# Optimization experiments

Hardware: AMD Instinct MI355X
Metric: run time of the kernel (lower is better)

## Reference

```python
import jax, jax.numpy as jnp
import numpy as np

N = 20000      # nodes
E = 640000     # edges (before self-loops)
NFEAT = 512
NHID = 128
HEADS = 2
NOUT = 64
K = 100
ALPHA = 0.2          # LeakyReLU negative slope
CLUSTER_TEMP = 5.0


def gat_layer(x, W, a_src, a_dst, b, src, dst, n, heads, out_c, neg_slope):
    """PyG-style GATConv (eval mode, self-loops already in src/dst).
    W: [heads*out_c, in_c], a_src/a_dst: [heads, out_c], b: [heads*out_c]."""
    h = (x @ W.T).reshape(n, heads, out_c)               # [N,H,C]
    alpha_src = (h * a_src[None]).sum(-1)                # [N,H]
    alpha_dst = (h * a_dst[None]).sum(-1)                # [N,H]
    e = alpha_src[src] + alpha_dst[dst]                  # [E',H]
    e = jnp.where(e > 0, e, neg_slope * e)               # LeakyReLU
    # segment softmax over incoming edges of each dst node
    m = jax.ops.segment_max(e, dst, num_segments=n)
    ex = jnp.exp(e - m[dst])
    s = jax.ops.segment_sum(ex, dst, num_segments=n)
    a = ex / (s[dst] + 1e-16)                            # [E',H]
    out = jax.ops.segment_sum(h[src] * a[:, :, None], dst, num_segments=n)
    return out.reshape(n, heads * out_c) + b


def cluster_iter(data_n, mu, num_iter, cluster_temp):
    """Soft k-means on row-normalized data. data_n: [N,D], mu: [K,D]."""
    def body(mu, _):
        dist = data_n @ mu.T                              # [N,K]
        r = jax.nn.softmax(cluster_temp * dist, axis=1)
        cluster_r = r.sum(axis=0)                         # [K]
        cluster_mean = r.T @ data_n                       # [K,D]
        return cluster_mean / cluster_r[:, None], None
    mu, _ = jax.lax.scan(body, mu, None, length=num_iter)
    dist = data_n @ mu.T
    r = jax.nn.softmax(cluster_temp * dist, axis=1)
    return mu, r, dist


def setup_inputs() -> dict:
    key = jax.random.key(0)
    ks = jax.random.split(key, 12)
    x = jax.random.normal(ks[0], (N, NFEAT), dtype=jnp.float32)
    edge_index = jax.random.randint(ks[1], (2, E), 0, N, dtype=jnp.int32)
    # GATConv layer 1 params
    W1 = jax.random.normal(ks[2], (HEADS * NHID, NFEAT), dtype=jnp.float32) * 0.05
    a_src1 = jax.random.normal(ks[3], (HEADS, NHID), dtype=jnp.float32) * 0.1
    a_dst1 = jax.random.normal(ks[4], (HEADS, NHID), dtype=jnp.float32) * 0.1
    b1 = jnp.zeros((HEADS * NHID,), dtype=jnp.float32)
    # GATConv layer 2 params (heads=1)
    W2 = jax.random.normal(ks[5], (NOUT, HEADS * NHID), dtype=jnp.float32) * 0.05
    a_src2 = jax.random.normal(ks[6], (1, NOUT), dtype=jnp.float32) * 0.1
    a_dst2 = jax.random.normal(ks[7], (1, NOUT), dtype=jnp.float32) * 0.1
    b2 = jnp.zeros((NOUT,), dtype=jnp.float32)
    # cluster init (self.init = torch.rand(K, nout))
    mu0 = jax.random.uniform(ks[8], (K, NOUT), dtype=jnp.float32)
    return {"x": x, "W1": W1, "a_src1": a_src1, "a_dst1": a_dst1, "b1": b1,
            "W2": W2, "a_src2": a_src2, "a_dst2": a_dst2, "b2": b2,
            "mu0": mu0, "edge_index": edge_index, "num_iter": 10}


def reference(x, W1, a_src1, a_dst1, b1, W2, a_src2, a_dst2, b2, mu0,
              edge_index, num_iter):
    loops = jnp.arange(N, dtype=edge_index.dtype)
    src = jnp.concatenate([edge_index[0], loops])
    dst = jnp.concatenate([edge_index[1], loops])
    h = jax.nn.elu(gat_layer(x, W1, a_src1, a_dst1, b1, src, dst,
                             N, HEADS, NHID, ALPHA))
    embeds = gat_layer(h, W2, a_src2, a_dst2, b2, src, dst,
                       N, 1, NOUT, ALPHA) + 1e-6
    data_n = embeds / jnp.linalg.norm(embeds, axis=1, keepdims=True)
    mu_init, _, _ = cluster_iter(data_n, mu0, num_iter, CLUSTER_TEMP)
    mu, r, dist = cluster_iter(data_n, jax.lax.stop_gradient(mu_init), 1,
                               CLUSTER_TEMP)
    return mu, r, embeds, dist
```

## Files before the change

### kernel.cpp

```cpp
#include <hip/hip_runtime.h>
#include <math.h>

#define Nn 20000
#define Ee 640000
#define ETOT 660000
#define NF 512
#define C1 256
#define C2 64
#define KC 100
#define TEMP 5.0f
#define NSLOPE 0.2f
#define NPART 250
#define CHB 80

__device__ __forceinline__ float wredSum(float v) {
#pragma unroll
  for (int off = 32; off > 0; off >>= 1) v += __shfl_xor(v, off, 64);
  return v;
}
__device__ __forceinline__ float wredMax(float v) {
#pragma unroll
  for (int off = 32; off > 0; off >>= 1) v = fmaxf(v, __shfl_xor(v, off, 64));
  return v;
}

__global__ void hist_kernel(const int* __restrict__ ei, int* __restrict__ deg) {
  int e = blockIdx.x * 256 + threadIdx.x;
  if (e >= ETOT) return;
  int dst = e < Ee ? ei[Ee + e] : e - Ee;
  atomicAdd(&deg[dst], 1);
}

__global__ __launch_bounds__(1024) void scan2_kernel(const int* __restrict__ deg,
    int* __restrict__ rowp, int* __restrict__ curs) {
  __shared__ int wsum[16];
  __shared__ int wpre[16];
  int t = threadIdx.x;
  int lane = t & 63, w = t >> 6;
  int loc[20];
  int tot = 0;
  int base = t * 20;
  if (t < 1000) {
#pragma unroll
    for (int i = 0; i < 20; i++) { tot += deg[base + i]; loc[i] = tot; }
  }
  int s = tot;
#pragma unroll
  for (int off = 1; off < 64; off <<= 1) {
    int u = __shfl_up(s, off, 64);
    if (lane >= off) s += u;
  }
  if (lane == 63) wsum[w] = s;
  __syncthreads();
  if (t == 0) {
    int c = 0;
#pragma unroll
    for (int i = 0; i < 16; i++) { c += wsum[i]; wpre[i] = c; }
    rowp[0] = 0;
  }
  __syncthreads();
  int p = (w > 0 ? wpre[w - 1] : 0) + s - tot;
  if (t < 1000) {
    int prev = 0;
#pragma unroll
    for (int i = 0; i < 20; i++) {
      rowp[base + i + 1] = p + loc[i];
      curs[base + i] = p + prev;
      prev = loc[i];
    }
  }
}

__global__ void scatter_kernel(const int* __restrict__ ei, int* __restrict__ curs,
                               int* __restrict__ ssort, int* __restrict__ dsort) {
  int e = blockIdx.x * 256 + threadIdx.x;
  if (e >= ETOT) return;
  int src = e < Ee ? ei[e] : e - Ee;
  int dst = e < Ee ? ei[Ee + e] : e - Ee;
  int pos = atomicAdd(&curs[dst], 1);
  ssort[pos] = src;
  dsort[pos] = dst;
}

__global__ __launch_bounds__(256) void edge_e1(const int* __restrict__ ssort,
    const int* __restrict__ dsort, const float* __restrict__ asn,
    const float* __restrict__ adn, float2* __restrict__ eb) {
  int i = blockIdx.x * 256 + threadIdx.x;
  if (i >= ETOT) return;
  int s = ssort[i], d = dsort[i];
  float2 a = ((const float2*)asn)[s];
  float2 b = ((const float2*)adn)[d];
  float e0 = a.x + b.x, e1 = a.y + b.y;
  e0 = e0 > 0.f ? e0 : NSLOPE * e0;
  e1 = e1 > 0.f ? e1 : NSLOPE * e1;
  eb[i] = make_float2(e0, e1);
}

__global__ __launch_bounds__(256) void edge_e2(const int* __restrict__ ssort,
    const int* __restrict__ dsort, const float* __restrict__ asn,
    const float* __restrict__ adn, float* __restrict__ eb) {
  int i = blockIdx.x * 256 + threadIdx.x;
  if (i >= ETOT) return;
  float e = asn[ssort[i]] + adn[dsort[i]];
  eb[i] = e > 0.f ? e : NSLOPE * e;
}

__global__ __launch_bounds__(256) void gemm128(const float* __restrict__ A,
    const float* __restrict__ B, float* __restrict__ C, int M, int N, int K) {
  __shared__ __align__(16) float As[16][132];
  __shared__ __align__(16) float Bs[16][132];
  int tid = threadIdx.x;
  int bm = blockIdx.x << 7, bn = blockIdx.y << 7;
  int tx = tid & 15, ty = tid >> 4;
  int r0 = tid >> 2;
  int c0 = (tid & 3) << 2;
  float acc[2][2][4][4] = {};
  for (int k0 = 0; k0 < K; k0 += 16) {
    float4 a0 = make_float4(0.f, 0.f, 0.f, 0.f), a1 = a0;
    int am0 = bm + r0, am1 = bm + 64 + r0;
    if (am0 < M) a0 = *(const float4*)(A + (size_t)am0 * K + k0 + c0);
    if (am1 < M) a1 = *(const float4*)(A + (size_t)am1 * K + k0 + c0);
    float4 b0 = *(const float4*)(B + (size_t)(bn + r0) * K + k0 + c0);
    float4 b1 = *(const float4*)(B + (size_t)(bn + 64 + r0) * K + k0 + c0);
    __syncthreads();
    As[c0 + 0][r0] = a0.x; As[c0 + 1][r0] = a0.y; As[c0 + 2][r0] = a0.z; As[c0 + 3][r0] = a0.w;
    As[c0 + 0][64 + r0] = a1.x; As[c0 + 1][64 + r0] = a1.y; As[c0 + 2][64 + r0] = a1.z; As[c0 + 3][64 + r0] = a1.w;
    Bs[c0 + 0][r0] = b0.x; Bs[c0 + 1][r0] = b0.y; Bs[c0 + 2][r0] = b0.z; Bs[c0 + 3][r0] = b0.w;
    Bs[c0 + 0][64 + r0] = b1.x; Bs[c0 + 1][64 + r0] = b1.y; Bs[c0 + 2][64 + r0] = b1.z; Bs[c0 + 3][64 + r0] = b1.w;
    __syncthreads();
#pragma unroll
    for (int k = 0; k < 16; k++) {
      float4 av0 = *(const float4*)&As[k][ty << 2];
      float4 av1 = *(const float4*)&As[k][64 + (ty << 2)];
      float4 bv0 = *(const float4*)&Bs[k][tx << 2];
      float4 bv1 = *(const float4*)&Bs[k][64 + (tx << 2)];
      float aa[2][4] = {{av0.x, av0.y, av0.z, av0.w}, {av1.x, av1.y, av1.z, av1.w}};
      float bb[2][4] = {{bv0.x, bv0.y, bv0.z, bv0.w}, {bv1.x, bv1.y, bv1.z, bv1.w}};
#pragma unroll
      for (int im = 0; im < 2; im++)
#pragma unroll
        for (int i = 0; i < 4; i++)
#pragma unroll
          for (int jn = 0; jn < 2; jn++)
#pragma unroll
            for (int j = 0; j < 4; j++)
              acc[im][jn][i][j] += aa[im][i] * bb[jn][j];
    }
  }
#pragma unroll
  for (int im = 0; im < 2; im++)
#pragma unroll
    for (int i = 0; i < 4; i++) {
      int row = bm + (im << 6) + (ty << 2) + i;
      if (row < M) {
#pragma unroll
        for (int jn = 0; jn < 2; jn++) {
          float4 v = make_float4(acc[im][jn][i][0], acc[im][jn][i][1],
                                 acc[im][jn][i][2], acc[im][jn][i][3]);
          *(float4*)(C + (size_t)row * N + bn + (jn << 6) + (tx << 2)) = v;
        }
      }
    }
}

__global__ __launch_bounds__(256) void gemm_nt(const float* __restrict__ A,
    const float* __restrict__ B, float* __restrict__ C, int M, int N, int K) {
  __shared__ __align__(16) float As[16][68];
  __shared__ __align__(16) float Bs[16][68];
  int tid = threadIdx.x;
  int bm = blockIdx.x << 6, bn = blockIdx.y << 6;
  int lr = tid >> 2;
  int lc = (tid & 3) << 2;
  int tx = tid & 15, ty = tid >> 4;
  float acc[4][4] = {};
  for (int k0 = 0; k0 < K; k0 += 16) {
    int am = bm + lr;
    float4 av = make_float4(0.f, 0.f, 0.f, 0.f);
    if (am < M) av = *(const float4*)(A + (size_t)am * K + k0 + lc);
    float4 bv = *(const float4*)(B + (size_t)(bn + lr) * K + k0 + lc);
    __syncthreads();
    As[lc + 0][lr] = av.x; As[lc + 1][lr] = av.y; As[lc + 2][lr] = av.z; As[lc + 3][lr] = av.w;
    Bs[lc + 0][lr] = bv.x; Bs[lc + 1][lr] = bv.y; Bs[lc + 2][lr] = bv.z; Bs[lc + 3][lr] = bv.w;
    __syncthreads();
#pragma unroll
    for (int k = 0; k < 16; k++) {
      float4 a = *(const float4*)&As[k][ty << 2];
      float4 b = *(const float4*)&Bs[k][tx << 2];
      float aa[4] = {a.x, a.y, a.z, a.w};
      float bb[4] = {b.x, b.y, b.z, b.w};
#pragma unroll
      for (int i = 0; i < 4; i++)
#pragma unroll
        for (int j = 0; j < 4; j++) acc[i][j] += aa[i] * bb[j];
    }
  }
#pragma unroll
  for (int i = 0; i < 4; i++) {
    int row = bm + (ty << 2) + i;
    if (row < M) {
#pragma unroll
      for (int j = 0; j < 4; j++)
        C[(size_t)row * N + bn + (tx << 2) + j] = acc[i][j];
    }
  }
}

__global__ __launch_bounds__(256) void alpha1_kernel(const float* __restrict__ h,
    const float* __restrict__ a_src, const float* __restrict__ a_dst,
    float* __restrict__ asn, float* __restrict__ adn) {
  int l = threadIdx.x & 63;
  int n = (blockIdx.x << 2) + (threadIdx.x >> 6);
  if (n >= Nn) return;
  const float* hr = h + (size_t)n * C1;
  float h0 = hr[l], h1v = hr[64 + l], h2v = hr[128 + l], h3v = hr[192 + l];
  float ps0 = h0 * a_src[l] + h1v * a_src[64 + l];
  float pd0 = h0 * a_dst[l] + h1v * a_dst[64 + l];
  float ps1 = h2v * a_src[128 + l] + h3v * a_src[192 + l];
  float pd1 = h2v * a_dst[128 + l] + h3v * a_dst[192 + l];
  ps0 = wredSum(ps0); pd0 = wredSum(pd0); ps1 = wredSum(ps1); pd1 = wredSum(pd1);
  if (l == 0) {
    asn[2 * n] = ps0; asn[2 * n + 1] = ps1;
    adn[2 * n] = pd0; adn[2 * n + 1] = pd1;
  }
}

__global__ __launch_bounds__(256) void alpha2_kernel(const float* __restrict__ h,
    const float* __restrict__ a_src, const float* __restrict__ a_dst,
    float* __restrict__ asn, float* __restrict__ adn) {
  int l = threadIdx.x & 63;
  int n = (blockIdx.x << 2) + (threadIdx.x >> 6);
  if (n >= Nn) return;
  float v = h[(size_t)n * C2 + l];
  float ps = wredSum(v * a_src[l]);
  float pd = wredSum(v * a_dst[l]);
  if (l == 0) { asn[n] = ps; adn[n] = pd; }
}

__global__ __launch_bounds__(256) void agg1_kernel(const float* __restrict__ h,
    const float2* __restrict__ eb, const int* __restrict__ ssort,
    const float* __restrict__ b1, const int* __restrict__ rowp,
    float* __restrict__ ho) {
  __shared__ float redm[8], reds[8];
  __shared__ __align__(16) float slab[4][256];
  int n = blockIdx.x, tid = threadIdx.x;
  int w = tid >> 6, l = tid & 63;
  int lo = rowp[n], hi = rowp[n + 1];
  float m0 = -1e30f, s0 = 0.f, m1 = -1e30f, s1 = 0.f;
  for (int i = lo + tid; i < hi; i += 256) {
    float2 e = eb[i];
    if (e.x > m0) { s0 = s0 * __expf(m0 - e.x) + 1.f; m0 = e.x; }
    else s0 += __expf(e.x - m0);
    if (e.y > m1) { s1 = s1 * __expf(m1 - e.y) + 1.f; m1 = e.y; }
    else s1 += __expf(e.y - m1);
  }
#pragma unroll
  for (int off = 32; off > 0; off >>= 1) {
    float om = __shfl_xor(m0, off, 64), os = __shfl_xor(s0, off, 64);
    float nm = fmaxf(m0, om);
    s0 = s0 * __expf(m0 - nm) + os * __expf(om - nm); m0 = nm;
    om = __shfl_xor(m1, off, 64); os = __shfl_xor(s1, off, 64);
    nm = fmaxf(m1, om);
    s1 = s1 * __expf(m1 - nm) + os * __expf(om - nm); m1 = nm;
  }
  if (l == 0) { redm[w] = m0; reds[w] = s0; redm[4 + w] = m1; reds[4 + w] = s1; }
  __syncthreads();
  float M0 = fmaxf(fmaxf(redm[0], redm[1]), fmaxf(redm[2], redm[3]));
  float M1 = fmaxf(fmaxf(redm[4], redm[5]), fmaxf(redm[6], redm[7]));
  float S0 = reds[0] * __expf(redm[0] - M0) + reds[1] * __expf(redm[1] - M0)
           + reds[2] * __expf(redm[2] - M0) + reds[3] * __expf(redm[3] - M0);
  float S1 = reds[4] * __expf(redm[4] - M1) + reds[5] * __expf(redm[5] - M1)
           + reds[6] * __expf(redm[6] - M1) + reds[7] * __expf(redm[7] - M1);
  float inv0 = 1.f / (S0 + 1e-16f), inv1 = 1.f / (S1 + 1e-16f);
  const bool lo_head = (l < 32);
  float Msel = lo_head ? M0 : M1;
  float isel = lo_head ? inv0 : inv1;
  int ch = l << 2;
  int deg = hi - lo;
  float4 accA = {0.f, 0.f, 0.f, 0.f}, accB = {0.f, 0.f, 0.f, 0.f};
  int j = w;
  for (; j + 4 < deg; j += 8) {
    int i0 = lo + j, i1 = lo + j + 4;
    float2 eA = eb[i0];
    float2 eB = eb[i1];
    int sA = ssort[i0], sB = ssort[i1];
    float4 ha = *(const float4*)(h + (size_t)sA * C1 + ch);
    float4 hb = *(const float4*)(h + (size_t)sB * C1 + ch);
    float wtA = __expf((lo_head ? eA.x : eA.y) - Msel) * isel;
    float wtB = __expf((lo_head ? eB.x : eB.y) - Msel) * isel;
    accA.x += wtA * ha.x; accA.y += wtA * ha.y; accA.z += wtA * ha.z; accA.w += wtA * ha.w;
    accB.x += wtB * hb.x; accB.y += wtB * hb.y; accB.z += wtB * hb.z; accB.w += wtB * hb.w;
  }
  if (j < deg) {
    int i0 = lo + j;
    float2 eA = eb[i0];
    int sA = ssort[i0];
    float4 ha = *(const float4*)(h + (size_t)sA * C1 + ch);
    float wtA = __expf((lo_head ? eA.x : eA.y) - Msel) * isel;
    accA.x += wtA * ha.x; accA.y += wtA * ha.y; accA.z += wtA * ha.z; accA.w += wtA * ha.w;
  }
  accA.x += accB.x; accA.y += accB.y; accA.z += accB.z; accA.w += accB.w;
  *(float4*)&slab[w][ch] = accA;
  __syncthreads();
  float v = slab[0][tid] + slab[1][tid] + slab[2][tid] + slab[3][tid] + b1[tid];
  ho[(size_t)n * C1 + tid] = v > 0.f ? v : __expf(v) - 1.0f;
}

__global__ __launch_bounds__(256) void agg2_kernel(const float* __restrict__ h,
    const float* __restrict__ eb, const int* __restrict__ ssort,
    const float* __restrict__ b2, const int* __restrict__ rowp,
    float* __restrict__ emb, float* __restrict__ dnrm) {
  int tid = threadIdx.x;
  int w = tid >> 6, l = tid & 63;
  int n = (blockIdx.x << 2) + w;
  int lo = rowp[n], hi = rowp[n + 1];
  float m = -1e30f, s = 0.f;
  for (int i = lo + l; i < hi; i += 64) {
    float e = eb[i];
    if (e > m) { s = s * __expf(m - e) + 1.f; m = e; }
    else s += __expf(e - m);
  }
#pragma unroll
  for (int off = 32; off > 0; off >>= 1) {
    float om = __shfl_xor(m, off, 64), os = __shfl_xor(s, off, 64);
    float nm = fmaxf(m, om);
    s = s * __expf(m - nm) + os * __expf(om - nm); m = nm;
  }
  float inv = 1.f / (s + 1e-16f);
  int g = l >> 4, lg = l & 15, ch = lg << 2;
  int deg = hi - lo;
  float4 accA = {0.f, 0.f, 0.f, 0.f}, accB = {0.f, 0.f, 0.f, 0.f};
  int j = g;
  for (; j + 4 < deg; j += 8) {
    int i0 = lo + j, i1 = lo + j + 4;
    float eA = eb[i0], eB = eb[i1];
    int sA = ssort[i0], sB = ssort[i1];
    float4 ha = *(const float4*)(h + (size_t)sA * C2 + ch);
    float4 hb = *(const float4*)(h + (size_t)sB * C2 + ch);
    float wtA = __expf(eA - m) * inv;
    float wtB = __expf(eB - m) * inv;
    accA.x += wtA * ha.x; accA.y += wtA * ha.y; accA.z += wtA * ha.z; accA.w += wtA * ha.w;
    accB.x += wtB * hb.x; accB.y += wtB * hb.y; accB.z += wtB * hb.z; accB.w += wtB * hb.w;
  }
  if (j < deg) {
    int i0 = lo + j;
    float eA = eb[i0];
    int sA = ssort[i0];
    float4 ha = *(const float4*)(h + (size_t)sA * C2 + ch);
    float wtA = __expf(eA - m) * inv;
    accA.x += wtA * ha.x; accA.y += wtA * ha.y; accA.z += wtA * ha.z; accA.w += wtA * ha.w;
  }
  accA.x += accB.x; accA.y += accB.y; accA.z += accB.z; accA.w += accB.w;
#pragma unroll
  for (int off = 16; off <= 32; off <<= 1) {
    accA.x += __shfl_xor(accA.x, off, 64);
    accA.y += __shfl_xor(accA.y, off, 64);
    accA.z += __shfl_xor(accA.z, off, 64);
    accA.w += __shfl_xor(accA.w, off, 64);
  }
  float4 bv = *(const float4*)(b2 + ch);
  float e0 = accA.x + bv.x + 1e-6f;
  float e1 = accA.y + bv.y + 1e-6f;
  float e2 = accA.z + bv.z + 1e-6f;
  float e3 = accA.w + bv.w + 1e-6f;
  float dot = e0 * e0 + e1 * e1 + e2 * e2 + e3 * e3;
#pragma unroll
  for (int off = 1; off < 16; off <<= 1) dot += __shfl_xor(dot, off, 64);
  float invn = 1.f / sqrtf(dot);
  if (g == 0) {
    *(float4*)(emb + (size_t)n * C2 + ch) = make_float4(e0, e1, e2, e3);
    *(float4*)(dnrm + (size_t)n * C2 + ch) =
        make_float4(e0 * invn, e1 * invn, e2 * invn, e3 * invn);
  }
}

template <int MODE>
__global__ __launch_bounds__(256) void fused_ac(
    const float* __restrict__ dnp, const float* __restrict__ mu_init,
    const float* __restrict__ mu, float* __restrict__ pcm, float* __restrict__ pcr,
    float* __restrict__ rout, float* __restrict__ distout,
    int it, const int* __restrict__ niter) {
  if (MODE == 0) { if (it > niter[0]) return; }
  __shared__ float mu_s[KC * 65];
  __shared__ __align__(16) float d_s[CHB * 68];
  __shared__ float r_s[CHB * KC];
  int tid = threadIdx.x, blk = blockIdx.x;
  const float* msrc = (MODE == 0 && it == 0) ? mu_init : mu;
  for (int idx = tid; idx < KC * 64; idx += 256)
    mu_s[(idx >> 6) * 65 + (idx & 63)] = msrc[idx];
  for (int idx = tid; idx < CHB * 64; idx += 256) {
    int row = idx >> 6, col = idx & 63;
    d_s[row * 68 + col] = dnp[(size_t)blk * (CHB * 64) + idx];
  }
  __syncthreads();
  int w = tid >> 6, l = tid & 63;
  const bool has2 = l < (KC - 64);
  int l2 = has2 ? 64 + l : l;
  for (int g = 0; g < 5; g++) {
    int nl0 = w * 20 + g * 4;
    float z1[4] = {0.f, 0.f, 0.f, 0.f}, z2[4] = {0.f, 0.f, 0.f, 0.f};
#pragma unroll 8
    for (int d = 0; d < 64; d++) {
      float m1v = mu_s[l * 65 + d];
      float m2v = mu_s[l2 * 65 + d];
#pragma unroll
      for (int nb = 0; nb < 4; nb++) {
        float dv = d_s[(nl0 + nb) * 68 + d];
        z1[nb] += m1v * dv;
        z2[nb] += m2v * dv;
      }
    }
#pragma unroll
    for (int nb = 0; nb < 4; nb++) {
      float g1 = TEMP * z1[nb];
      float g2 = has2 ? TEMP * z2[nb] : -1e30f;
      float m = wredMax(fmaxf(g1, g2));
      float e1 = expf(g1 - m);
      float e2 = has2 ? expf(g2 - m) : 0.f;
      float inv = 1.0f / wredSum(e1 + e2);
      int nl = nl0 + nb;
      if (MODE == 0) {
        r_s[nl * KC + l] = e1 * inv;
        if (has2) r_s[nl * KC + 64 + l] = e2 * inv;
      } else {
        size_t n = (size_t)blk * CHB + nl;
        rout[n * KC + l] = e1 * inv;
        if (has2) rout[n * KC + 64 + l] = e2 * inv;
        distout[n * KC + l] = z1[nb];
        if (has2) distout[n * KC + 64 + l] = z2[nb];
      }
    }
  }
  if (MODE == 0) {
    __syncthreads();
    int tx = tid & 15, ky = tid >> 4;
    float acc[7][4] = {};
    float accr[7] = {};
    for (int j = 0; j < CHB; j++) {
      float4 dv = *(const float4*)&d_s[j * 68 + (tx << 2)];
#pragma unroll
      for (int jj = 0; jj < 7; jj++) {
        int kk = ky + (jj << 4);
        if (kk < KC) {
          float rv = r_s[j * KC + kk];
          acc[jj][0] += rv * dv.x; acc[jj][1] += rv * dv.y;
          acc[jj][2] += rv * dv.z; acc[jj][3] += rv * dv.w;
          if (tx == 0) accr[jj] += rv;
        }
      }
    }
#pragma unroll
    for (int jj = 0; jj < 7; jj++) {
      int kk = ky + (jj << 4);
      if (kk < KC) {
        float* p = pcm + (size_t)blk * 6400 + kk * 64 + (tx << 2);
        p[0] = acc[jj][0]; p[1] = acc[jj][1]; p[2] = acc[jj][2]; p[3] = acc[jj][3];
        if (tx == 0) pcr[blk * KC + kk] = accr[jj];
      }
    }
  }
}

__global__ __launch_bounds__(256) void muupd_kernel(const float* __restrict__ pcm,
    const float* __restrict__ pcr, float* __restrict__ mu,
    int it, const int* __restrict__ niter) {
  if (it > niter[0]) return;
  __shared__ float part[4][64];
  __shared__ float red[4];
  int k = blockIdx.x, tid = threadIdx.x;
  int d = tid & 63, bg = tid >> 6;
  float s = 0.f;
  for (int b = bg; b < NPART; b += 4)
    s += pcm[(size_t)b * 6400 + k * 64 + d];
  part[bg][d] = s;
  float c = (tid < NPART) ? pcr[tid * KC + k] : 0.f;
  c = wredSum(c);
  if ((tid & 63) == 0) red[tid >> 6] = c;
  __syncthreads();
  if (tid < 64) {
    float cr = red[0] + red[1] + red[2] + red[3];
    mu[k * 64 + tid] = (part[0][tid] + part[1][tid] + part[2][tid] + part[3][tid]) / cr;
  }
}

__global__ void copy_f(const float* __restrict__ a, float* __restrict__ b, int n) {
  int i = blockIdx.x * 256 + threadIdx.x;
  if (i < n) b[i] = a[i];
}

extern "C" void kernel_launch(void* const* d_in, const int* in_sizes, int n_in,
                              void* d_out, int out_size, void* d_ws, size_t ws_size,
                              hipStream_t stream) {
  const float* x    = (const float*)d_in[0];
  const float* W1   = (const float*)d_in[1];
  const float* asr1 = (const float*)d_in[2];
  const float* ads1 = (const float*)d_in[3];
  const float* b1   = (const float*)d_in[4];
  const float* W2   = (const float*)d_in[5];
  const float* asr2 = (const float*)d_in[6];
  const float* ads2 = (const float*)d_in[7];
  const float* b2   = (const float*)d_in[8];
  const float* mu0  = (const float*)d_in[9];
  const int*   ei   = (const int*)d_in[10];
  const int*   nit  = (const int*)d_in[11];

  float* f = (float*)d_ws;
  float* h1   = f;  f += (size_t)Nn * C1;
  float* h1o  = f;  f += (size_t)Nn * C1;
  float* as1  = f;  f += Nn * 2;
  float* ad1  = f;  f += Nn * 2;
  float* h2   = f;  f += (size_t)Nn * C2;
  float* as2  = f;  f += Nn;
  float* ad2  = f;  f += Nn;
  float* dn   = f;  f += (size_t)Nn * C2;
  float* pcm  = f;  f += (size_t)NPART * 6400;
  float* pcr  = f;  f += NPART * KC;
  float* mu   = f;  f += KC * C2;
  float2* ebA = (float2*)f; f += (size_t)ETOT * 2;
  float* ebB  = (float*)ebA;
  int* ip = (int*)f;
  int* deg   = ip;  ip += Nn;
  int* rowp  = ip;  ip += Nn + 1;
  int* curs  = ip;  ip += Nn;
  int* ssort = ip;  ip += ETOT;
  int* dsort = ip;  ip += ETOT;

  float* out_mu = (float*)d_out;
  float* out_r  = out_mu + KC * C2;
  float* out_e  = out_r + (size_t)Nn * KC;
  float* out_d  = out_e + (size_t)Nn * C2;

  hipMemsetAsync(deg, 0, Nn * sizeof(int), stream);
  hist_kernel<<<(ETOT + 255) / 256, 256, 0, stream>>>(ei, deg);
  scan2_kernel<<<1, 1024, 0, stream>>>(deg, rowp, curs);
  scatter_kernel<<<(ETOT + 255) / 256, 256, 0, stream>>>(ei, curs, ssort, dsort);

  gemm128<<<dim3(157, 2), 256, 0, stream>>>(x, W1, h1, Nn, C1, NF);
  alpha1_kernel<<<5000, 256, 0, stream>>>(h1, asr1, ads1, as1, ad1);
  edge_e1<<<(ETOT + 255) / 256, 256, 0, stream>>>(ssort, dsort, as1, ad1, ebA);
  agg1_kernel<<<Nn, 256, 0, stream>>>(h1, ebA, ssort, b1, rowp, h1o);

  gemm_nt<<<dim3(313, 1), 256, 0, stream>>>(h1o, W2, h2, Nn, C2, C1);
  alpha2_kernel<<<5000, 256, 0, stream>>>(h2, asr2, ads2, as2, ad2);
  edge_e2<<<(ETOT + 255) / 256, 256, 0, stream>>>(ssort, dsort, as2, ad2, ebB);
  agg2_kernel<<<5000, 256, 0, stream>>>(h2, ebB, ssort, b2, rowp, out_e, dn);

  for (int it = 0; it < 12; it++) {
    fused_ac<0><<<NPART, 256, 0, stream>>>(dn, mu0, mu, pcm, pcr, nullptr, nullptr, it, nit);
    muupd_kernel<<<KC, 256, 0, stream>>>(pcm, pcr, mu, it, nit);
  }
  fused_ac<1><<<NPART, 256, 0, stream>>>(dn, mu0, mu, nullptr, nullptr, out_r, out_d, 0, nit);
  copy_f<<<25, 256, 0, stream>>>(mu, out_mu, KC * C2);
}
```

Measured before the change: 1.146 ms.

## Use split-bf16 MFMA for first GEMM and fuse clustering into cooperative kernel

The first-layer FP32 SIMT GEMM is replaced with a bf16 MFMA GEMM that splits each operand into high and low bf16 parts and runs three MFMA products to approximate FP32 accuracy. Separately, the soft k-means loop of 25 kernel launches (fused assign/accumulate, mu update, final pass, copy) becomes one cooperative kernel that uses grid syncs between the partial-sum and mu-update phases and keeps the data chunk resident in LDS. This aims to cut launch overhead, repeated data reloads, and GEMM compute time. It risks a small accuracy loss from the bf16 split and depends on all 250 blocks being co-resident for the cooperative launch.

```diff
diff --git a/kernel.cpp b/kernel.cpp
--- a/kernel.cpp
+++ b/kernel.cpp
@@ -1,5 +1,9 @@
 #include <hip/hip_runtime.h>
+#include <hip/hip_bf16.h>
+#include <hip/hip_cooperative_groups.h>
 #include <math.h>
+
+namespace cg = cooperative_groups;
 
 #define Nn 20000
 #define Ee 640000
@@ -13,6 +17,9 @@
 #define NPART 250
 #define CHB 80
 
+typedef __attribute__((ext_vector_type(8))) short bf16x8;
+typedef __attribute__((ext_vector_type(4))) float f32x4;
+
 __device__ __forceinline__ float wredSum(float v) {
 #pragma unroll
   for (int off = 32; off > 0; off >>= 1) v += __shfl_xor(v, off, 64);
@@ -22,6 +29,14 @@
 #pragma unroll
   for (int off = 32; off > 0; off >>= 1) v = fmaxf(v, __shfl_xor(v, off, 64));
   return v;
+}
+__device__ __forceinline__ ushort f2bf(float f) {
+  __hip_bfloat16 b = __float2bfloat16(f);
+  return *(ushort*)&b;
+}
+__device__ __forceinline__ float bf2f(ushort u) {
+  __hip_bfloat16 b = *(__hip_bfloat16*)&u;
+  return __bfloat162float(b);
 }
 
 __global__ void hist_kernel(const int* __restrict__ ei, int* __restrict__ deg) {
@@ -105,62 +120,80 @@
   eb[i] = e > 0.f ? e : NSLOPE * e;
 }
 
-__global__ __launch_bounds__(256) void gemm128(const float* __restrict__ A,
-    const float* __restrict__ B, float* __restrict__ C, int M, int N, int K) {
-  __shared__ __align__(16) float As[16][132];
-  __shared__ __align__(16) float Bs[16][132];
+__global__ __launch_bounds__(256) void gemm1_mfma(const float* __restrict__ A,
+    const float* __restrict__ B, float* __restrict__ C) {
+  __shared__ ushort Ah[128 * 40], Al[128 * 40], Bh[128 * 40], Bl[128 * 40];
   int tid = threadIdx.x;
   int bm = blockIdx.x << 7, bn = blockIdx.y << 7;
-  int tx = tid & 15, ty = tid >> 4;
-  int r0 = tid >> 2;
-  int c0 = (tid & 3) << 2;
-  float acc[2][2][4][4] = {};
-  for (int k0 = 0; k0 < K; k0 += 16) {
-    float4 a0 = make_float4(0.f, 0.f, 0.f, 0.f), a1 = a0;
-    int am0 = bm + r0, am1 = bm + 64 + r0;
-    if (am0 < M) a0 = *(const float4*)(A + (size_t)am0 * K + k0 + c0);
-    if (am1 < M) a1 = *(const float4*)(A + (size_t)am1 * K + k0 + c0);
-    float4 b0 = *(const float4*)(B + (size_t)(bn + r0) * K + k0 + c0);
-    float4 b1 = *(const float4*)(B + (size_t)(bn + 64 + r0) * K + k0 + c0);
+  int w = tid >> 6, lane = tid & 63;
+  int wm = (w >> 1) << 6, wn = (w & 1) << 6;
+  int fr = lane & 15, ko = (lane >> 4) << 3;
+  f32x4 acc[4][4] = {};
+  for (int k0 = 0; k0 < 512; k0 += 32) {
     __syncthreads();
-    As[c0 + 0][r0] = a0.x; As[c0 + 1][r0] = a0.y; As[c0 + 2][r0] = a0.z; As[c0 + 3][r0] = a0.w;
-    As[c0 + 0][64 + r0] = a1.x; As[c0 + 1][64 + r0] = a1.y; As[c0 + 2][64 + r0] = a1.z; As[c0 + 3][64 + r0] = a1.w;
-    Bs[c0 + 0][r0] = b0.x; Bs[c0 + 1][r0] = b0.y; Bs[c0 + 2][r0] = b0.z; Bs[c0 + 3][r0] = b0.w;
-    Bs[c0 + 0][64 + r0] = b1.x; Bs[c0 + 1][64 + r0] = b1.y; Bs[c0 + 2][64 + r0] = b1.z; Bs[c0 + 3][64 + r0] = b1.w;
+#pragma unroll
+    for (int cc = 0; cc < 4; cc++) {
+      int c = tid + (cc << 8);
+      int row = c >> 3, q = c & 7;
+      int off = row * 40 + (q << 2);
+      int gr = bm + row;
+      float4 va = (gr < Nn) ? *(const float4*)(A + (size_t)gr * NF + k0 + (q << 2))
+                            : make_float4(0.f, 0.f, 0.f, 0.f);
+      float4 vb = *(const float4*)(B + (size_t)(bn + row) * NF + k0 + (q << 2));
+      ushort h0 = f2bf(va.x), h1 = f2bf(va.y), h2 = f2bf(va.z), h3 = f2bf(va.w);
+      *(ushort4*)&Ah[off] = make_ushort4(h0, h1, h2, h3);
+      *(ushort4*)&Al[off] = make_ushort4(
+          f2bf(va.x - bf2f(h0)), f2bf(va.y - bf2f(h1)),
+          f2bf(va.z - bf2f(h2)), f2bf(va.w - bf2f(h3)));
+      ushort g0 = f2bf(vb.x), g1 = f2bf(vb.y), g2 = f2bf(vb.z), g3 = f2bf(vb.w);
+      *(ushort4*)&Bh[off] = make_ushort4(g0, g1, g2, g3);
+      *(ushort4*)&Bl[off] = make_ushort4(
+          f2bf(vb.x - bf2f(g0)), f2bf(vb.y - bf2f(g1)),
+          f2bf(vb.z - bf2f(g2)), f2bf(vb.w - bf2f(g3)));
+    }
     __syncthreads();
-#pragma unroll
-    for (int k = 0; k < 16; k++) {
-      float4 av0 = *(const float4*)&As[k][ty << 2];
-      float4 av1 = *(const float4*)&As[k][64 + (ty << 2)];
-      float4 bv0 = *(const float4*)&Bs[k][tx << 2];
-      float4 bv1 = *(const float4*)&Bs[k][64 + (tx << 2)];
-      float aa[2][4] = {{av0.x, av0.y, av0.z, av0.w}, {av1.x, av1.y, av1.z, av1.w}};
-      float bb[2][4] = {{bv0.x, bv0.y, bv0.z, bv0.w}, {bv1.x, bv1.y, bv1.z, bv1.w}};
-#pragma unroll
-      for (int im = 0; im < 2; im++)
-#pragma unroll
-        for (int i = 0; i < 4; i++)
-#pragma unroll
-          for (int jn = 0; jn < 2; jn++)
-#pragma unroll
-            for (int j = 0; j < 4; j++)
-              acc[im][jn][i][j] += aa[im][i] * bb[jn][j];
-    }
-  }
-#pragma unroll
-  for (int im = 0; im < 2; im++)
-#pragma unroll
-    for (int i = 0; i < 4; i++) {
-      int row = bm + (im << 6) + (ty << 2) + i;
-      if (row < M) {
-#pragma unroll
-        for (int jn = 0; jn < 2; jn++) {
-          float4 v = make_float4(acc[im][jn][i][0], acc[im][jn][i][1],
-                                 acc[im][jn][i][2], acc[im][jn][i][3]);
-          *(float4*)(C + (size_t)row * N + bn + (jn << 6) + (tx << 2)) = v;
-        }
+    bf16x8 aH[4], bH[4], t[4];
+#pragma unroll
+    for (int mf = 0; mf < 4; mf++)
+      aH[mf] = *(const bf16x8*)&Ah[(wm + (mf << 4) + fr) * 40 + ko];
+#pragma unroll
+    for (int nf = 0; nf < 4; nf++)
+      bH[nf] = *(const bf16x8*)&Bh[(wn + (nf << 4) + fr) * 40 + ko];
+#pragma unroll
+    for (int mf = 0; mf < 4; mf++)
+#pragma unroll
+      for (int nf = 0; nf < 4; nf++)
+        acc[mf][nf] = __builtin_amdgcn_mfma_f32_16x16x32_bf16(aH[mf], bH[nf], acc[mf][nf], 0, 0, 0);
+#pragma unroll
+    for (int nf = 0; nf < 4; nf++)
+      t[nf] = *(const bf16x8*)&Bl[(wn + (nf << 4) + fr) * 40 + ko];
+#pragma unroll
+    for (int mf = 0; mf < 4; mf++)
+#pragma unroll
+      for (int nf = 0; nf < 4; nf++)
+        acc[mf][nf] = __builtin_amdgcn_mfma_f32_16x16x32_bf16(aH[mf], t[nf], acc[mf][nf], 0, 0, 0);
+#pragma unroll
+    for (int mf = 0; mf < 4; mf++)
+      t[mf] = *(const bf16x8*)&Al[(wm + (mf << 4) + fr) * 40 + ko];
+#pragma unroll
+    for (int mf = 0; mf < 4; mf++)
+#pragma unroll
+      for (int nf = 0; nf < 4; nf++)
+        acc[mf][nf] = __builtin_amdgcn_mfma_f32_16x16x32_bf16(t[mf], bH[nf], acc[mf][nf], 0, 0, 0);
+  }
+  int cr = (lane >> 4) << 2, cc2 = lane & 15;
+#pragma unroll
+  for (int mf = 0; mf < 4; mf++) {
+#pragma unroll
+    for (int r = 0; r < 4; r++) {
+      int row = bm + wm + (mf << 4) + cr + r;
+      if (row < Nn) {
+#pragma unroll
+        for (int nf = 0; nf < 4; nf++)
+          C[(size_t)row * C1 + bn + wn + (nf << 4) + cc2] = acc[mf][nf][r];
       }
     }
+  }
 }
 
 __global__ __launch_bounds__(256) void gemm_nt(const float* __restrict__ A,
@@ -373,28 +406,105 @@
   }
 }
 
-template <int MODE>
-__global__ __launch_bounds__(256) void fused_ac(
-    const float* __restrict__ dnp, const float* __restrict__ mu_init,
-    const float* __restrict__ mu, float* __restrict__ pcm, float* __restrict__ pcr,
-    float* __restrict__ rout, float* __restrict__ distout,
-    int it, const int* __restrict__ niter) {
-  if (MODE == 0) { if (it > niter[0]) return; }
+__global__ __launch_bounds__(256) void coop_cluster(
+    const float* __restrict__ dnp, const float* __restrict__ mu0,
+    float* __restrict__ mu, float* __restrict__ pcm, float* __restrict__ pcr,
+    float* __restrict__ out_mu, float* __restrict__ out_r, float* __restrict__ out_d,
+    const int* __restrict__ niter) {
+  cg::grid_group gg = cg::this_grid();
   __shared__ float mu_s[KC * 65];
   __shared__ __align__(16) float d_s[CHB * 68];
   __shared__ float r_s[CHB * KC];
+  __shared__ float part[4][64];
+  __shared__ float redc[4];
   int tid = threadIdx.x, blk = blockIdx.x;
-  const float* msrc = (MODE == 0 && it == 0) ? mu_init : mu;
-  for (int idx = tid; idx < KC * 64; idx += 256)
-    mu_s[(idx >> 6) * 65 + (idx & 63)] = msrc[idx];
-  for (int idx = tid; idx < CHB * 64; idx += 256) {
-    int row = idx >> 6, col = idx & 63;
-    d_s[row * 68 + col] = dnp[(size_t)blk * (CHB * 64) + idx];
-  }
-  __syncthreads();
   int w = tid >> 6, l = tid & 63;
   const bool has2 = l < (KC - 64);
   int l2 = has2 ? 64 + l : l;
+  for (int idx = tid; idx < CHB * 64; idx += 256)
+    d_s[(idx >> 6) * 68 + (idx & 63)] = dnp[(size_t)blk * (CHB * 64) + idx];
+  for (int idx = tid; idx < KC * 64; idx += 256)
+    mu_s[(idx >> 6) * 65 + (idx & 63)] = mu0[idx];
+  __syncthreads();
+  int NI = niter[0];
+  for (int it = 0; it <= NI; ++it) {
+    for (int g = 0; g < 5; g++) {
+      int nl0 = w * 20 + g * 4;
+      float z1[4] = {0.f, 0.f, 0.f, 0.f}, z2[4] = {0.f, 0.f, 0.f, 0.f};
+#pragma unroll 8
+      for (int d = 0; d < 64; d++) {
+        float m1v = mu_s[l * 65 + d];
+        float m2v = mu_s[l2 * 65 + d];
+#pragma unroll
+        for (int nb = 0; nb < 4; nb++) {
+          float dv = d_s[(nl0 + nb) * 68 + d];
+          z1[nb] += m1v * dv;
+          z2[nb] += m2v * dv;
+        }
+      }
+#pragma unroll
+      for (int nb = 0; nb < 4; nb++) {
+        float g1 = TEMP * z1[nb];
+        float g2 = has2 ? TEMP * z2[nb] : -1e30f;
+        float m = wredMax(fmaxf(g1, g2));
+        float e1 = expf(g1 - m);
+        float e2 = has2 ? expf(g2 - m) : 0.f;
+        float inv = 1.0f / wredSum(e1 + e2);
+        int nl = nl0 + nb;
+        r_s[nl * KC + l] = e1 * inv;
+        if (has2) r_s[nl * KC + 64 + l] = e2 * inv;
+      }
+    }
+    __syncthreads();
+    {
+      int tx = tid & 15, ky = tid >> 4;
+      float acc[7][4] = {};
+      float accr[7] = {};
+      for (int j = 0; j < CHB; j++) {
+        float4 dv = *(const float4*)&d_s[j * 68 + (tx << 2)];
+#pragma unroll
+        for (int jj = 0; jj < 7; jj++) {
+          int kk = ky + (jj << 4);
+          if (kk < KC) {
+            float rv = r_s[j * KC + kk];
+            acc[jj][0] += rv * dv.x; acc[jj][1] += rv * dv.y;
+            acc[jj][2] += rv * dv.z; acc[jj][3] += rv * dv.w;
+            if (tx == 0) accr[jj] += rv;
+          }
+        }
+      }
+#pragma unroll
+      for (int jj = 0; jj < 7; jj++) {
+        int kk = ky + (jj << 4);
+        if (kk < KC) {
+          float* p = pcm + (size_t)blk * 6400 + kk * 64 + (tx << 2);
+          p[0] = acc[jj][0]; p[1] = acc[jj][1]; p[2] = acc[jj][2]; p[3] = acc[jj][3];
+          if (tx == 0) pcr[blk * KC + kk] = accr[jj];
+        }
+      }
+    }
+    gg.sync();
+    if (blk < KC) {
+      int k = blk;
+      int d = tid & 63, bg = tid >> 6;
+      float s = 0.f;
+      for (int b = bg; b < NPART; b += 4)
+        s += pcm[(size_t)b * 6400 + k * 64 + d];
+      part[bg][d] = s;
+      float c = (tid < NPART) ? pcr[tid * KC + k] : 0.f;
+      c = wredSum(c);
+      if (l == 0) redc[w] = c;
+      __syncthreads();
+      if (tid < 64) {
+        float cr = redc[0] + redc[1] + redc[2] + redc[3];
+        mu[k * 64 + tid] = (part[0][tid] + part[1][tid] + part[2][tid] + part[3][tid]) / cr;
+      }
+    }
+    gg.sync();
+    for (int idx = tid; idx < KC * 64; idx += 256)
+      mu_s[(idx >> 6) * 65 + (idx & 63)] = mu[idx];
+    __syncthreads();
+  }
   for (int g = 0; g < 5; g++) {
     int nl0 = w * 20 + g * 4;
     float z1[4] = {0.f, 0.f, 0.f, 0.f}, z2[4] = {0.f, 0.f, 0.f, 0.f};
@@ -417,74 +527,17 @@
       float e1 = expf(g1 - m);
       float e2 = has2 ? expf(g2 - m) : 0.f;
       float inv = 1.0f / wredSum(e1 + e2);
-      int nl = nl0 + nb;
-      if (MODE == 0) {
-        r_s[nl * KC + l] = e1 * inv;
-        if (has2) r_s[nl * KC + 64 + l] = e2 * inv;
-      } else {
-        size_t n = (size_t)blk * CHB + nl;
-        rout[n * KC + l] = e1 * inv;
-        if (has2) rout[n * KC + 64 + l] = e2 * inv;
-        distout[n * KC + l] = z1[nb];
-        if (has2) distout[n * KC + 64 + l] = z2[nb];
-      }
-    }
-  }
-  if (MODE == 0) {
-    __syncthreads();
-    int tx = tid & 15, ky = tid >> 4;
-    float acc[7][4] = {};
-    float accr[7] = {};
-    for (int j = 0; j < CHB; j++) {
-      float4 dv = *(const float4*)&d_s[j * 68 + (tx << 2)];
-#pragma unroll
-      for (int jj = 0; jj < 7; jj++) {
-        int kk = ky + (jj << 4);
-        if (kk < KC) {
-          float rv = r_s[j * KC + kk];
-          acc[jj][0] += rv * dv.x; acc[jj][1] += rv * dv.y;
-          acc[jj][2] += rv * dv.z; acc[jj][3] += rv * dv.w;
-          if (tx == 0) accr[jj] += rv;
-        }
-      }
-    }
-#pragma unroll
-    for (int jj = 0; jj < 7; jj++) {
-      int kk = ky + (jj << 4);
-      if (kk < KC) {
-        float* p = pcm + (size_t)blk * 6400 + kk * 64 + (tx << 2);
-        p[0] = acc[jj][0]; p[1] = acc[jj][1]; p[2] = acc[jj][2]; p[3] = acc[jj][3];
-        if (tx == 0) pcr[blk * KC + kk] = accr[jj];
-      }
-    }
-  }
-}
-
-__global__ __launch_bounds__(256) void muupd_kernel(const float* __restrict__ pcm,
-    const float* __restrict__ pcr, float* __restrict__ mu,
-    int it, const int* __restrict__ niter) {
-  if (it > niter[0]) return;
-  __shared__ float part[4][64];
-  __shared__ float red[4];
-  int k = blockIdx.x, tid = threadIdx.x;
-  int d = tid & 63, bg = tid >> 6;
-  float s = 0.f;
-  for (int b = bg; b < NPART; b += 4)
-    s += pcm[(size_t)b * 6400 + k * 64 + d];
-  part[bg][d] = s;
-  float c = (tid < NPART) ? pcr[tid * KC + k] : 0.f;
-  c = wredSum(c);
-  if ((tid & 63) == 0) red[tid >> 6] = c;
-  __syncthreads();
-  if (tid < 64) {
-    float cr = red[0] + red[1] + red[2] + red[3];
-    mu[k * 64 + tid] = (part[0][tid] + part[1][tid] + part[2][tid] + part[3][tid]) / cr;
-  }
-}
-
-__global__ void copy_f(const float* __restrict__ a, float* __restrict__ b, int n) {
-  int i = blockIdx.x * 256 + threadIdx.x;
-  if (i < n) b[i] = a[i];
+      size_t n = (size_t)blk * CHB + nl0 + nb;
+      out_r[n * KC + l] = e1 * inv;
+      if (has2) out_r[n * KC + 64 + l] = e2 * inv;
+      out_d[n * KC + l] = z1[nb];
+      if (has2) out_d[n * KC + 64 + l] = z2[nb];
+    }
+  }
+  if (blk == 0) {
+    for (int idx = tid; idx < KC * 64; idx += 256)
+      out_mu[idx] = mu_s[(idx >> 6) * 65 + (idx & 63)];
+  }
 }
 
 extern "C" void kernel_launch(void* const* d_in, const int* in_sizes, int n_in,
@@ -534,7 +587,7 @@
   scan2_kernel<<<1, 1024, 0, stream>>>(deg, rowp, curs);
   scatter_kernel<<<(ETOT + 255) / 256, 256, 0, stream>>>(ei, curs, ssort, dsort);
 
-  gemm128<<<dim3(157, 2), 256, 0, stream>>>(x, W1, h1, Nn, C1, NF);
+  gemm1_mfma<<<dim3(157, 2), 256, 0, stream>>>(x, W1, h1);
   alpha1_kernel<<<5000, 256, 0, stream>>>(h1, asr1, ads1, as1, ad1);
   edge_e1<<<(ETOT + 255) / 256, 256, 0, stream>>>(ssort, dsort, as1, ad1, ebA);
   agg1_kernel<<<Nn, 256, 0, stream>>>(h1, ebA, ssort, b1, rowp, h1o);
@@ -544,10 +597,7 @@
   edge_e2<<<(ETOT + 255) / 256, 256, 0, stream>>>(ssort, dsort, as2, ad2, ebB);
   agg2_kernel<<<5000, 256, 0, stream>>>(h2, ebB, ssort, b2, rowp, out_e, dn);
 
-  for (int it = 0; it < 12; it++) {
-    fused_ac<0><<<NPART, 256, 0, stream>>>(dn, mu0, mu, pcm, pcr, nullptr, nullptr, it, nit);
-    muupd_kernel<<<KC, 256, 0, stream>>>(pcm, pcr, mu, it, nit);
-  }
-  fused_ac<1><<<NPART, 256, 0, stream>>>(dn, mu0, mu, nullptr, nullptr, out_r, out_d, 0, nit);
-  copy_f<<<25, 256, 0, stream>>>(mu, out_mu, KC * C2);
-}
+  void* cargs[] = {(void*)&dn, (void*)&mu0, (void*)&mu, (void*)&pcm, (void*)&pcr,
+                   (void*)&out_mu, (void*)&out_r, (void*)&out_d, (void*)&nit};
+  hipLaunchCooperativeKernel((void*)coop_cluster, dim3(NPART), dim3(256), cargs, 0, stream);
+}
```

New measurement: 1.672 ms. 45.9% more time.
